# Optimization experiments

Hardware: AMD Instinct MI355X
Metric: run time of the kernel (lower is better)

Reference implementation:

```python
import jax, jax.numpy as jnp
import numpy as np

B, T, C = 2, 2048, 2048
H, HK = 16, 4          # n_head, n_kv_head (GQA)
HD = C // H            # head_dim = 128
EPS = 1e-6             # rms-norm eps


def _rope(x, cos, sin):
    # x: [B,T,h,d]; cos/sin: [T, d/2] (rotate-half RoPE)
    d2 = x.shape[-1] // 2
    x1, x2 = x[..., :d2], x[..., d2:]
    c = cos[None, :, None, :]
    s = sin[None, :, None, :]
    return jnp.concatenate([x1 * c - x2 * s, x1 * s + x2 * c], axis=-1)


def _rms(x):
    # weightless QK-norm (F.rms_norm over last dim)
    return x * jax.lax.rsqrt(jnp.mean(x * x, axis=-1, keepdims=True) + EPS)


def setup_inputs() -> dict:
    key = jax.random.key(0)
    ks = jax.random.split(key, 6)
    x = jax.random.normal(ks[0], (B, T, C), dtype=jnp.float32)
    # realistic RoPE tables
    inv_freq = 1.0 / (10000.0 ** (jnp.arange(0, HD, 2, dtype=jnp.float32) / HD))  # [HD/2]
    ang = jnp.arange(T, dtype=jnp.float32)[:, None] * inv_freq[None, :]           # [T, HD/2]
    cos, sin = jnp.cos(ang), jnp.sin(ang)
    std = 0.02
    Wq = jax.random.normal(ks[1], (C, H * HD), dtype=jnp.float32) * std
    Wk = jax.random.normal(ks[2], (C, HK * HD), dtype=jnp.float32) * std
    Wv = jax.random.normal(ks[3], (C, HK * HD), dtype=jnp.float32) * std
    Wproj = jax.random.normal(ks[4], (C, C), dtype=jnp.float32) * std
    mix1 = jnp.float32(1.0)
    mix2 = jnp.float32(0.5)
    return {"x": x, "cos": cos, "sin": sin, "Wq": Wq, "Wk": Wk, "Wv": Wv,
            "Wproj": Wproj, "mix1": mix1, "mix2": mix2}


def reference(x, cos, sin, Wq, Wk, Wv, Wproj, mix1, mix2):
    Bx, Tx, Cx = x.shape
    q = (x @ Wq).reshape(Bx, Tx, H, HD)
    k = (x @ Wk).reshape(Bx, Tx, HK, HD)
    v = (x @ Wv).reshape(Bx, Tx, HK, HD)
    q = _rms(_rope(q, cos, sin))
    k = _rms(_rope(k, cos, sin))
    q = q.transpose(0, 2, 1, 3)  # [B,H,T,D]
    k = k.transpose(0, 2, 1, 3)  # [B,HK,T,D]
    v = v.transpose(0, 2, 1, 3)
    rep = H // HK
    k = jnp.repeat(k, rep, axis=1)  # GQA repeat -> [B,H,T,D]
    v = jnp.repeat(v, rep, axis=1)
    att = jnp.einsum('bhqd,bhkd->bhqk', q, k) * (1.0 / np.sqrt(HD))
    mask = jnp.tril(jnp.ones((Tx, Tx), dtype=bool))
    att = jnp.where(mask[None, None], att, -jnp.inf)
    att = jax.nn.softmax(att, axis=-1)
    y1 = att @ v            # first-order attention output
    y2 = att @ y1           # second-order simplicial mixing (reuses att)
    y = mix1 * y1 + mix2 * y2
    y = y.transpose(0, 2, 1, 3).reshape(Bx, Tx, Cx)
    return y @ Wproj
```

## Files before the change

### kernel.cpp

```cpp
#include <hip/hip_runtime.h>
#include <hip/hip_bf16.h>
#include <cstdint>
#include <cstddef>

#define AS1 __attribute__((address_space(1)))
#define AS3 __attribute__((address_space(3)))

typedef __attribute__((ext_vector_type(8))) short bf16x8;
typedef __attribute__((ext_vector_type(4))) float f32x4;

__device__ __forceinline__ void gload_lds16(const void* g, void* l) {
  __builtin_amdgcn_global_load_lds((const AS1 void*)g, (AS3 void*)l, 16, 0, 0);
}

#define MFMA_BF16(A, B, C) __builtin_amdgcn_mfma_f32_16x16x32_bf16((A), (B), (C), 0, 0, 0)

#define QSCALE 0.12751744f

__device__ __forceinline__ uint32_t pk2(float a, float b) {
  uint32_t ua = (uint32_t)__builtin_bit_cast(unsigned short, __float2bfloat16(a));
  uint32_t ub = (uint32_t)__builtin_bit_cast(unsigned short, __float2bfloat16(b));
  return ua | (ub << 16);
}
__device__ __forceinline__ float b2f(unsigned short u) {
  return __builtin_bit_cast(float, (uint32_t)u << 16);
}

__device__ __forceinline__ float red8_sum(float v) {
  int x;
  x = __builtin_amdgcn_update_dpp(0, __builtin_bit_cast(int, v), 0xB1, 0xF, 0xF, true);
  v += __builtin_bit_cast(float, x);
  x = __builtin_amdgcn_update_dpp(0, __builtin_bit_cast(int, v), 0x4E, 0xF, 0xF, true);
  v += __builtin_bit_cast(float, x);
  x = __builtin_amdgcn_update_dpp(0, __builtin_bit_cast(int, v), 0x141, 0xF, 0xF, true);
  v += __builtin_bit_cast(float, x);
  return v;
}

__global__ __launch_bounds__(256) void prep_kernel(const float* __restrict__ x,
                                                   __hip_bfloat16* __restrict__ xb,
                                                   const float* __restrict__ Wq,
                                                   const float* __restrict__ Wk,
                                                   const float* __restrict__ Wv,
                                                   const float* __restrict__ Wp,
                                                   __hip_bfloat16* __restrict__ WTa,
                                                   __hip_bfloat16* __restrict__ WpT) {
  __shared__ float tile[32][33];
  int id = blockIdx.x;
  int tx = threadIdx.x, ty = threadIdx.y;
  if (id < 8192) {
    int i = id * 256 + ty * 32 + tx;
    float4 v = ((const float4*)x)[i];
    __hip_bfloat16* o = xb + (size_t)i * 4;
    o[0] = __float2bfloat16(v.x);
    o[1] = __float2bfloat16(v.y);
    o[2] = __float2bfloat16(v.z);
    o[3] = __float2bfloat16(v.w);
    return;
  }
  id -= 8192;
  const float* in; __hip_bfloat16* out; int is, os, bx, by;
  if (id < 4096)      { in = Wq; out = WTa;                          is = 2048; os = 2048; bx = id & 63; by = id >> 6; }
  else if (id < 5120) { int t = id - 4096; in = Wk; out = WTa + (size_t)2048 * 2048; is = 512; os = 2048; bx = t & 15; by = t >> 4; }
  else if (id < 6144) { int t = id - 5120; in = Wv; out = WTa + (size_t)2560 * 2048; is = 512; os = 2048; bx = t & 15; by = t >> 4; }
  else                { int t = id - 6144; in = Wp; out = WpT;       is = 2048; os = 2048; bx = t & 63; by = t >> 6; }
  int c0 = bx * 32, r0 = by * 32;
#pragma unroll
  for (int i = 0; i < 32; i += 8)
    tile[ty + i][tx] = in[(size_t)(r0 + ty + i) * is + c0 + tx];
  __syncthreads();
#pragma unroll
  for (int i = 0; i < 32; i += 8)
    out[(size_t)(c0 + ty + i) * os + r0 + tx] = __float2bfloat16(tile[tx][ty + i]);
}

__global__ __launch_bounds__(256, 2) void gemm_qkv_rope_kernel(
    const __hip_bfloat16* __restrict__ A,
    const __hip_bfloat16* __restrict__ Bt,
    const float* __restrict__ cosb,
    const float* __restrict__ sinb,
    __hip_bfloat16* __restrict__ qT,
    __hip_bfloat16* __restrict__ kT,
    __hip_bfloat16* __restrict__ vt) {
  __shared__ __align__(16) char smem[65536];
  __hip_bfloat16* CL4 = (__hip_bfloat16*)smem;
  const int K = 2048;
  const int tid = threadIdx.x;
  const int lane = tid & 63;
  const int wid = tid >> 6;
  const int wm = wid >> 1, wn = wid & 1;
  const int bid = blockIdx.x;
  const int swz = (bid & 7) * 96 + (bid >> 3);
  const int tm = swz / 24, tn = swz % 24;
  const int row0 = tm << 7, col0 = tn << 7;
  const int fr = lane & 15, hi = lane >> 4;

  auto STAGE = [&](int buf, int k0) {
#pragma unroll
    for (int i = 0; i < 4; ++i) {
      int f = i * 256 + tid;
      int r = f >> 3, s = f & 7, sx = s ^ (r & 7);
      gload_lds16(A + (size_t)(row0 + r) * K + k0 + sx * 8,
                  smem + buf * 16384 + f * 16);
    }
#pragma unroll
    for (int i = 0; i < 4; ++i) {
      int f = i * 256 + tid;
      int r = f >> 3, s = f & 7, sx = s ^ (r & 7);
      gload_lds16(Bt + (size_t)(col0 + r) * K + k0 + sx * 8,
                  smem + 32768 + buf * 16384 + f * 16);
    }
  };

  f32x4 acc[4][4] = {};
  STAGE(0, 0);
  int cur = 0;
  for (int kk = 0; kk < 32; ++kk) {
    if (kk > 0) __builtin_amdgcn_s_barrier();
    __builtin_amdgcn_sched_barrier(0);
    if (kk + 1 < 32) STAGE(cur ^ 1, (kk + 1) * 64);
    __builtin_amdgcn_sched_barrier(0);
    if (kk + 1 < 32) asm volatile("s_waitcnt vmcnt(8)" ::: "memory");
    else             asm volatile("s_waitcnt vmcnt(0)" ::: "memory");
    __builtin_amdgcn_s_barrier();
    __builtin_amdgcn_sched_barrier(0);
    const char* Ac = smem + cur * 16384;
    const char* Bc = smem + 32768 + cur * 16384;
#pragma unroll
    for (int kh = 0; kh < 2; ++kh) {
      bf16x8 af[4], bfr[4];
#pragma unroll
      for (int n = 0; n < 4; ++n) {
        int rowb = wn * 64 + n * 16 + fr;
        int sl = (kh * 4 + hi) ^ (rowb & 7);
        bfr[n] = *(const bf16x8*)(Bc + rowb * 128 + sl * 16);
      }
#pragma unroll
      for (int m = 0; m < 4; ++m) {
        int rowa = wm * 64 + m * 16 + fr;
        int sl = (kh * 4 + hi) ^ (rowa & 7);
        af[m] = *(const bf16x8*)(Ac + rowa * 128 + sl * 16);
      }
      __builtin_amdgcn_s_setprio(1);
#pragma unroll
      for (int m = 0; m < 4; ++m)
#pragma unroll
        for (int n = 0; n < 4; ++n)
          acc[m][n] = MFMA_BF16(af[m], bfr[n], acc[m][n]);
      __builtin_amdgcn_s_setprio(0);
    }
    cur ^= 1;
  }
  __syncthreads();

#pragma unroll
  for (int m = 0; m < 4; ++m)
#pragma unroll
    for (int n = 0; n < 4; ++n) {
      int q4 = wm * 16 + m * 4 + hi;
      int col = wn * 64 + n * 16 + fr;
      *(uint2*)(CL4 + ((q4 * 133 + col) << 2)) =
          make_uint2(pk2(acc[m][n][0], acc[m][n][1]), pk2(acc[m][n][2], acc[m][n][3]));
    }
  __syncthreads();

  const int b = row0 >> 11;
  const int t0 = row0 & 2047;

  if (col0 >= 2560) {
    const int hv = (col0 - 2560) >> 7;
    __hip_bfloat16* vb = vt + (size_t)(b * 4 + hv) * 128 * 2048;
    const int col = tid >> 1, th = tid & 1;
    uint2 w[16];
#pragma unroll
    for (int qq = 0; qq < 16; ++qq)
      w[qq] = *(const uint2*)(CL4 + (((th * 16 + qq) * 133 + col) << 2));
    __hip_bfloat16* dstv = vb + (size_t)col * 2048 + t0 + th * 64;
#pragma unroll
    for (int e = 0; e < 8; ++e)
      *(uint4*)(dstv + e * 8) = make_uint4(w[2 * e].x, w[2 * e].y, w[2 * e + 1].x, w[2 * e + 1].y);
    return;
  }

  const int quad = tid >> 3, cp = tid & 7;
  const int tb = t0 + quad * 4;
  bf16x8 lov[4], hiv[4];
#pragma unroll
  for (int e = 0; e < 4; ++e) {
    lov[e] = *(const bf16x8*)(CL4 + ((quad * 133 + cp * 8 + e * 2) << 2));
    hiv[e] = *(const bf16x8*)(CL4 + ((quad * 133 + 64 + cp * 8 + e * 2) << 2));
  }
  const float oscale = (col0 < 2048) ? QSCALE : 1.0f;
  __hip_bfloat16* dstq = (col0 < 2048)
      ? qT + (size_t)(b * 16 + (col0 >> 7)) * 2048 * 128
      : kT + (size_t)(b * 4 + ((col0 - 2048) >> 7)) * 2048 * 128;

  float o1v[4][8], o2v[4][8], ssum[4];
#pragma unroll
  for (int rr = 0; rr < 4; ++rr) {
    const float* cb = cosb + (size_t)(tb + rr) * 64 + cp * 8;
    const float* sb = sinb + (size_t)(tb + rr) * 64 + cp * 8;
    float4 c0 = *(const float4*)cb, c1 = *(const float4*)(cb + 4);
    float4 s0 = *(const float4*)sb, s1 = *(const float4*)(sb + 4);
    float cc[8] = {c0.x, c0.y, c0.z, c0.w, c1.x, c1.y, c1.z, c1.w};
    float sn[8] = {s0.x, s0.y, s0.z, s0.w, s1.x, s1.y, s1.z, s1.w};
    float ss = 0.f;
#pragma unroll
    for (int e = 0; e < 4; ++e)
#pragma unroll
      for (int w2 = 0; w2 < 2; ++w2) {
        int pd = e * 2 + w2;
        float x1 = b2f((unsigned short)lov[e][w2 * 4 + rr]);
        float x2 = b2f((unsigned short)hiv[e][w2 * 4 + rr]);
        float a = x1 * cc[pd] - x2 * sn[pd];
        float bb = x1 * sn[pd] + x2 * cc[pd];
        o1v[rr][pd] = a;
        o2v[rr][pd] = bb;
        ss += a * a + bb * bb;
      }
    ssum[rr] = ss;
  }
#pragma unroll
  for (int rr = 0; rr < 4; ++rr) {
    float rn = rsqrtf(red8_sum(ssum[rr]) * (1.f / 128.f) + 1e-6f) * oscale;
    __hip_bfloat16* dr = dstq + (size_t)(tb + rr) * 128 + cp * 8;
    *(uint4*)dr = make_uint4(pk2(o1v[rr][0] * rn, o1v[rr][1] * rn),
                             pk2(o1v[rr][2] * rn, o1v[rr][3] * rn),
                             pk2(o1v[rr][4] * rn, o1v[rr][5] * rn),
                             pk2(o1v[rr][6] * rn, o1v[rr][7] * rn));
    *(uint4*)(dr + 64) = make_uint4(pk2(o2v[rr][0] * rn, o2v[rr][1] * rn),
                                    pk2(o2v[rr][2] * rn, o2v[rr][3] * rn),
                                    pk2(o2v[rr][4] * rn, o2v[rr][5] * rn),
                                    pk2(o2v[rr][6] * rn, o2v[rr][7] * rn));
  }
}

__global__ __launch_bounds__(256) void gemm_bf16_kernel(const __hip_bfloat16* __restrict__ A,
                                                        const __hip_bfloat16* __restrict__ Bt,
                                                        float* __restrict__ C,
                                                        int M, int N, int K) {
  __shared__ __align__(16) char smem[32768];
  const int tid = threadIdx.x;
  const int lane = tid & 63;
  const int wid = tid >> 6;
  const int wm = wid >> 1, wn = wid & 1;
  const int nwg = gridDim.x;
  const int bid = blockIdx.x;
  const int swz = (bid & 7) * (nwg >> 3) + (bid >> 3);
  const int ntile = N >> 7;
  const int tm = swz / ntile, tn = swz % ntile;
  const int row0 = tm << 7, col0 = tn << 7;

  const int fr = lane & 15;
  const int kg = (lane >> 4) * 8;

  auto STAGE = [&](int buf, int k0) {
#pragma unroll
    for (int i = 0; i < 2; ++i) {
      int f = i * 256 + tid;
      int r = f >> 2, s = f & 3;
      gload_lds16(A + (size_t)(row0 + r) * K + k0 + s * 8,
                  smem + buf * 8192 + (i * 256 + wid * 64) * 16);
      gload_lds16(Bt + (size_t)(col0 + r) * K + k0 + s * 8,
                  smem + 16384 + buf * 8192 + (i * 256 + wid * 64) * 16);
    }
  };

  f32x4 acc[4][4] = {};
  const int nk = K >> 5;
  STAGE(0, 0);
  int cur = 0;
  for (int kk = 0; kk < nk; ++kk) {
    if (kk > 0) __builtin_amdgcn_s_barrier();
    __builtin_amdgcn_sched_barrier(0);
    if (kk + 1 < nk) STAGE(cur ^ 1, (kk + 1) * 32);
    __builtin_amdgcn_sched_barrier(0);
    if (kk + 1 < nk) asm volatile("s_waitcnt vmcnt(4)" ::: "memory");
    else             asm volatile("s_waitcnt vmcnt(0)" ::: "memory");
    __builtin_amdgcn_s_barrier();
    __builtin_amdgcn_sched_barrier(0);
    const __hip_bfloat16* Ac = (const __hip_bfloat16*)(smem + cur * 8192);
    const __hip_bfloat16* Bc = (const __hip_bfloat16*)(smem + 16384 + cur * 8192);
    bf16x8 af[4], bfr[4];
#pragma unroll
    for (int m = 0; m < 4; ++m)
      af[m] = *(const bf16x8*)(Ac + (wm * 64 + m * 16 + fr) * 32 + kg);
#pragma unroll
    for (int n = 0; n < 4; ++n)
      bfr[n] = *(const bf16x8*)(Bc + (wn * 64 + n * 16 + fr) * 32 + kg);
#pragma unroll
    for (int m = 0; m < 4; ++m)
#pragma unroll
      for (int n = 0; n < 4; ++n)
        acc[m][n] = MFMA_BF16(af[m], bfr[n], acc[m][n]);
    cur ^= 1;
  }

  const int cr = (lane >> 4) * 4;
#pragma unroll
  for (int m = 0; m < 4; ++m)
#pragma unroll
    for (int n = 0; n < 4; ++n) {
      int col = col0 + wn * 64 + n * 16 + fr;
#pragma unroll
      for (int r = 0; r < 4; ++r) {
        int row = row0 + wm * 64 + m * 16 + cr + r;
        C[(size_t)row * N + col] = acc[m][n][r];
      }
    }
}


__global__ __launch_bounds__(256, 2) void attn_pass1_kernel(
    const __hip_bfloat16* __restrict__ qT,
    const __hip_bfloat16* __restrict__ kT,
    const __hip_bfloat16* __restrict__ vt,
    __hip_bfloat16* __restrict__ y1u,
    float* __restrict__ Mb,
    float* __restrict__ Lb,
    const float* __restrict__ mix1p,
    const float* __restrict__ mix2p) {
  __shared__ __align__(16) __hip_bfloat16 Ks[2][64 * 128];
  __shared__ __align__(16) __hip_bfloat16 Vs[2][128 * 64];
  __shared__ __align__(16) char Ps[4][32 * 128];
  const int tid = threadIdx.x, lane = tid & 63, wid = tid >> 6;
  const int bi = blockIdx.x;
  const int u = bi & 255, half = bi >> 8;
  const int g = u & 7;
  const int pslot = (u >> 3) & 7;
  const int bh = g * 4 + (u >> 6);
  const int j = half ? (15 - pslot) : pslot;
  const int q0 = j * 128;
  const int nt = 2 * j + 2;
  const int sd = 2 * j + (wid >> 1);
  const __hip_bfloat16* Kp = kT + (size_t)g * 2048 * 128;
  const __hip_bfloat16* Vp = vt + (size_t)g * 128 * 2048;
  const int fr = lane & 15, hi = lane >> 4;

  bf16x8 qf[2][4];
  {
    const __hip_bfloat16* Qp = qT + ((size_t)bh * 2048 + q0 + wid * 32) * 128;
#pragma unroll
    for (int rr = 0; rr < 2; ++rr)
#pragma unroll
      for (int dc = 0; dc < 4; ++dc)
        qf[rr][dc] = *(const bf16x8*)(Qp + (rr * 16 + fr) * 128 + dc * 32 + hi * 8);
  }

  f32x4 accO[2][8] = {};
  float m[2], l[2];
  m[0] = m[1] = -1e30f; l[0] = l[1] = 0.f;

  char* Pb = Ps[wid];

  auto STAGE = [&](int buf, int kt) {
    const int k0 = kt * 64;
#pragma unroll
    for (int i = 0; i < 4; ++i) {
      int f = i * 256 + tid;
      int r = f >> 4, s = f & 15, sx = s ^ (r & 7);
      gload_lds16(Kp + (size_t)(k0 + r) * 128 + sx * 8,
                  (char*)Ks[buf] + (i * 256 + wid * 64) * 16);
    }
#pragma unroll
    for (int i = 0; i < 4; ++i) {
      int f = i * 256 + tid;
      int r = f >> 3, s = f & 7, sx = s ^ (r & 7);
      gload_lds16(Vp + (size_t)r * 2048 + k0 + sx * 8,
                  (char*)Vs[buf] + (i * 256 + wid * 64) * 16);
    }
  };

  STAGE(0, 0);
  int cur = 0;
  for (int s = 0; s < nt; ++s) {
    if (s > 0) __builtin_amdgcn_s_barrier();
    __builtin_amdgcn_sched_barrier(0);
    if (s + 1 < nt) STAGE(cur ^ 1, s + 1);
    __builtin_amdgcn_sched_barrier(0);
    if (s + 1 < nt) asm volatile("s_waitcnt vmcnt(8)" ::: "memory");
    else            asm volatile("s_waitcnt vmcnt(0)" ::: "memory");
    __builtin_amdgcn_s_barrier();
    __builtin_amdgcn_sched_barrier(0);

    const bool active = (s <= sd);
    if (active) {
      const char* Kc = (const char*)Ks[cur];
      f32x4 sf[2][4] = {};
      __builtin_amdgcn_s_setprio(1);
#pragma unroll
      for (int c = 0; c < 4; ++c) {
        const int krow = c * 16 + fr;
#pragma unroll
        for (int dc = 0; dc < 4; ++dc) {
          int slot = (dc * 4 + hi) ^ (krow & 7);
          bf16x8 kf = *(const bf16x8*)(Kc + krow * 256 + slot * 16);
          sf[0][c] = MFMA_BF16(kf, qf[0][dc], sf[0][c]);
          sf[1][c] = MFMA_BF16(kf, qf[1][dc], sf[1][c]);
        }
      }
      __builtin_amdgcn_s_setprio(0);
      float lmax[2];
#pragma unroll
      for (int rr = 0; rr < 2; ++rr) {
        if (s == sd) {
          const int qq = q0 + wid * 32 + rr * 16 + fr;
#pragma unroll
          for (int c = 0; c < 4; ++c) {
            const int kb = s * 64 + c * 16 + hi * 4;
#pragma unroll
            for (int r = 0; r < 4; ++r)
              if (kb + r > qq) sf[rr][c][r] = -1e30f;
          }
        }
        float v = -1e30f;
#pragma unroll
        for (int c = 0; c < 4; ++c)
#pragma unroll
          for (int r = 0; r < 4; ++r) v = fmaxf(v, sf[rr][c][r]);
        lmax[rr] = v;
      }
      bool grow = (lmax[0] > m[0] + 8.f) | (lmax[1] > m[1] + 8.f);
      if (__any(grow)) {
        float a[2];
#pragma unroll
        for (int rr = 0; rr < 2; ++rr) {
          float v = lmax[rr];
          v = fmaxf(v, __shfl_xor(v, 16));
          v = fmaxf(v, __shfl_xor(v, 32));
          float mn = fmaxf(m[rr], v);
          a[rr] = __builtin_amdgcn_exp2f(m[rr] - mn);
          m[rr] = mn;
          l[rr] *= a[rr];
        }
#pragma unroll
        for (int rr = 0; rr < 2; ++rr)
#pragma unroll
          for (int r = 0; r < 4; ++r) {
            float aq = __shfl(a[rr], hi * 4 + r);
#pragma unroll
            for (int f = 0; f < 8; ++f) accO[rr][f][r] *= aq;
          }
      }
#pragma unroll
      for (int rr = 0; rr < 2; ++rr) {
        float rs = 0.f;
#pragma unroll
        for (int c = 0; c < 4; ++c)
#pragma unroll
          for (int r = 0; r < 4; ++r) {
            float p = __builtin_amdgcn_exp2f(sf[rr][c][r] - m[rr]);
            sf[rr][c][r] = p;
            rs += p;
          }
        l[rr] += rs;
      }
#pragma unroll
      for (int rr = 0; rr < 2; ++rr) {
        const int row = rr * 16 + fr;
        char* Prow = Pb + row * 128;
#pragma unroll
        for (int c = 0; c < 4; ++c) {
          uint32_t w0 = pk2(sf[rr][c][0], sf[rr][c][1]);
          uint32_t w1 = pk2(sf[rr][c][2], sf[rr][c][3]);
          int sl = (c * 2 + (hi >> 1)) ^ (row & 7);
          *(uint2*)(Prow + sl * 16 + (hi & 1) * 8) = make_uint2(w0, w1);
        }
      }
      bf16x8 pf[2][2];
#pragma unroll
      for (int rr = 0; rr < 2; ++rr) {
        const int row = rr * 16 + fr;
#pragma unroll
        for (int kc = 0; kc < 2; ++kc) {
          int sl = (kc * 4 + hi) ^ (row & 7);
          pf[rr][kc] = *(const bf16x8*)(Pb + row * 128 + sl * 16);
        }
      }
      const __hip_bfloat16* Vc = Vs[cur];
      __builtin_amdgcn_s_setprio(1);
#pragma unroll
      for (int kc = 0; kc < 2; ++kc)
#pragma unroll
        for (int f = 0; f < 8; ++f) {
          int vrow = f * 16 + fr;
          int vslot = (kc * 4 + hi) ^ (fr & 7);
          bf16x8 vf = *(const bf16x8*)(Vc + vrow * 64 + vslot * 8);
          accO[0][f] = MFMA_BF16(pf[0][kc], vf, accO[0][f]);
          accO[1][f] = MFMA_BF16(pf[1][kc], vf, accO[1][f]);
        }
      __builtin_amdgcn_s_setprio(0);
    }
    cur ^= 1;
  }

  float lsum[2];
#pragma unroll
  for (int rr = 0; rr < 2; ++rr) {
    float v = l[rr];
    v += __shfl_xor(v, 16);
    v += __shfl_xor(v, 32);
    lsum[rr] = v;
  }
  const float m1v = mix1p[0], m2v = mix2p[0];
  float rlq[2][4];
#pragma unroll
  for (int rr = 0; rr < 2; ++rr) {
    float inv = 1.f / lsum[rr];
#pragma unroll
    for (int r = 0; r < 4; ++r) rlq[rr][r] = __shfl(inv, hi * 4 + r);
  }
  const int t0 = q0 + wid * 32;
#pragma unroll
  for (int rr = 0; rr < 2; ++rr) {
    const int tb = t0 + rr * 16 + hi * 4;
#pragma unroll
    for (int f = 0; f < 8; ++f) {
      const int d = f * 16 + fr;
      const ushort4 v4 = *(const ushort4*)(vt + ((size_t)g * 128 + d) * 2048 + tb);
      float u0 = m1v * b2f(v4.x) + m2v * (accO[rr][f][0] * rlq[rr][0]);
      float u1 = m1v * b2f(v4.y) + m2v * (accO[rr][f][1] * rlq[rr][1]);
      float u2 = m1v * b2f(v4.z) + m2v * (accO[rr][f][2] * rlq[rr][2]);
      float u3 = m1v * b2f(v4.w) + m2v * (accO[rr][f][3] * rlq[rr][3]);
      *(uint2*)(y1u + ((size_t)bh * 128 + d) * 2048 + tb) =
          make_uint2(pk2(u0, u1), pk2(u2, u3));
    }
  }
  if (hi == 0) {
#pragma unroll
    for (int rr = 0; rr < 2; ++rr) {
      Mb[(size_t)bh * 2048 + t0 + rr * 16 + fr] = m[rr];
      Lb[(size_t)bh * 2048 + t0 + rr * 16 + fr] = lsum[rr];
    }
  }
}

__global__ __launch_bounds__(256, 2) void attn_pass2_kernel(
    const __hip_bfloat16* __restrict__ qT,
    const __hip_bfloat16* __restrict__ kT,
    const __hip_bfloat16* __restrict__ y1u,
    const float* __restrict__ Mb,
    const float* __restrict__ Lb,
    __hip_bfloat16* __restrict__ ymix) {
  __shared__ __align__(16) __hip_bfloat16 Ks[2][64 * 128];
  __shared__ __align__(16) __hip_bfloat16 Vs[2][128 * 64];
  __shared__ __align__(16) char Ps[4][32 * 128];
  const int tid = threadIdx.x, lane = tid & 63, wid = tid >> 6;
  const int bi = blockIdx.x;
  const int u = bi & 255, half = bi >> 8;
  const int g = u & 7;
  const int pslot = (u >> 3) & 7;
  const int bh = g * 4 + (u >> 6);
  const int h = bh & 15, b = bh >> 4;
  const int j = half ? (15 - pslot) : pslot;
  const int q0 = j * 128;
  const int nt = 2 * j + 2;
  const int sd = 2 * j + (wid >> 1);
  const __hip_bfloat16* Kp = kT + (size_t)g * 2048 * 128;
  const __hip_bfloat16* Yp = y1u + (size_t)bh * 128 * 2048;
  const int fr = lane & 15, hi = lane >> 4;

  bf16x8 qf[2][4];
  float mr[2], rl[2];
  {
    const __hip_bfloat16* Qp = qT + ((size_t)bh * 2048 + q0 + wid * 32) * 128;
#pragma unroll
    for (int rr = 0; rr < 2; ++rr)
#pragma unroll
      for (int dc = 0; dc < 4; ++dc)
        qf[rr][dc] = *(const bf16x8*)(Qp + (rr * 16 + fr) * 128 + dc * 32 + hi * 8);
    const size_t qb = (size_t)bh * 2048 + q0 + wid * 32;
    mr[0] = Mb[qb + fr];        mr[1] = Mb[qb + 16 + fr];
    rl[0] = 1.f / Lb[qb + fr];  rl[1] = 1.f / Lb[qb + 16 + fr];
  }

  f32x4 accO[2][8] = {};
  char* Pb = Ps[wid];

  auto STAGE = [&](int buf, int kt) {
    const int k0 = kt * 64;
#pragma unroll
    for (int i = 0; i < 4; ++i) {
      int f = i * 256 + tid;
      int r = f >> 4, s = f & 15, sx = s ^ (r & 7);
      gload_lds16(Kp + (size_t)(k0 + r) * 128 + sx * 8,
                  (char*)Ks[buf] + (i * 256 + wid * 64) * 16);
    }
#pragma unroll
    for (int i = 0; i < 4; ++i) {
      int f = i * 256 + tid;
      int r = f >> 3, s = f & 7, sx = s ^ (r & 7);
      gload_lds16(Yp + (size_t)r * 2048 + k0 + sx * 8,
                  (char*)Vs[buf] + (i * 256 + wid * 64) * 16);
    }
  };

  STAGE(0, 0);
  int cur = 0;
  for (int s = 0; s < nt; ++s) {
    if (s > 0) __builtin_amdgcn_s_barrier();
    __builtin_amdgcn_sched_barrier(0);
    if (s + 1 < nt) STAGE(cur ^ 1, s + 1);
    __builtin_amdgcn_sched_barrier(0);
    if (s + 1 < nt) asm volatile("s_waitcnt vmcnt(8)" ::: "memory");
    else            asm volatile("s_waitcnt vmcnt(0)" ::: "memory");
    __builtin_amdgcn_s_barrier();
    __builtin_amdgcn_sched_barrier(0);

    const bool active = (s <= sd);
    if (active) {
      const char* Kc = (const char*)Ks[cur];
      f32x4 sf[2][4] = {};
      __builtin_amdgcn_s_setprio(1);
#pragma unroll
      for (int c = 0; c < 4; ++c) {
        const int krow = c * 16 + fr;
#pragma unroll
        for (int dc = 0; dc < 4; ++dc) {
          int slot = (dc * 4 + hi) ^ (krow & 7);
          bf16x8 kf = *(const bf16x8*)(Kc + krow * 256 + slot * 16);
          sf[0][c] = MFMA_BF16(kf, qf[0][dc], sf[0][c]);
          sf[1][c] = MFMA_BF16(kf, qf[1][dc], sf[1][c]);
        }
      }
      __builtin_amdgcn_s_setprio(0);
#pragma unroll
      for (int rr = 0; rr < 2; ++rr) {
        if (s == sd) {
          const int qq = q0 + wid * 32 + rr * 16 + fr;
#pragma unroll
          for (int c = 0; c < 4; ++c) {
            const int kb = s * 64 + c * 16 + hi * 4;
#pragma unroll
            for (int r = 0; r < 4; ++r)
              if (kb + r > qq) sf[rr][c][r] = -1e30f;
          }
        }
#pragma unroll
        for (int c = 0; c < 4; ++c)
#pragma unroll
          for (int r = 0; r < 4; ++r)
            sf[rr][c][r] = __builtin_amdgcn_exp2f(sf[rr][c][r] - mr[rr]) * rl[rr];
      }
#pragma unroll
      for (int rr = 0; rr < 2; ++rr) {
        const int row = rr * 16 + fr;
        char* Prow = Pb + row * 128;
#pragma unroll
        for (int c = 0; c < 4; ++c) {
          uint32_t w0 = pk2(sf[rr][c][0], sf[rr][c][1]);
          uint32_t w1 = pk2(sf[rr][c][2], sf[rr][c][3]);
          int sl = (c * 2 + (hi >> 1)) ^ (row & 7);
          *(uint2*)(Prow + sl * 16 + (hi & 1) * 8) = make_uint2(w0, w1);
        }
      }
      bf16x8 pf[2][2];
#pragma unroll
      for (int rr = 0; rr < 2; ++rr) {
        const int row = rr * 16 + fr;
#pragma unroll
        for (int kc = 0; kc < 2; ++kc) {
          int sl = (kc * 4 + hi) ^ (row & 7);
          pf[rr][kc] = *(const bf16x8*)(Pb + row * 128 + sl * 16);
        }
      }
      const __hip_bfloat16* Vc = Vs[cur];
      __builtin_amdgcn_s_setprio(1);
#pragma unroll
      for (int kc = 0; kc < 2; ++kc)
#pragma unroll
        for (int f = 0; f < 8; ++f) {
          int vrow = f * 16 + fr;
          int vslot = (kc * 4 + hi) ^ (fr & 7);
          bf16x8 vf = *(const bf16x8*)(Vc + vrow * 64 + vslot * 8);
          accO[0][f] = MFMA_BF16(pf[0][kc], vf, accO[0][f]);
          accO[1][f] = MFMA_BF16(pf[1][kc], vf, accO[1][f]);
        }
      __builtin_amdgcn_s_setprio(0);
    }
    cur ^= 1;
  }

#pragma unroll
  for (int rr = 0; rr < 2; ++rr) {
#pragma unroll
    for (int f = 0; f < 8; ++f) {
      const int d = f * 16 + fr;
#pragma unroll
      for (int r = 0; r < 4; ++r) {
        int q = q0 + wid * 32 + rr * 16 + hi * 4 + r;
        ymix[((size_t)b * 2048 + q) * 2048 + h * 128 + d] = __float2bfloat16(accO[rr][f][r]);
      }
    }
  }
}

extern "C" void kernel_launch(void* const* d_in, const int* in_sizes, int n_in,
                              void* d_out, int out_size, void* d_ws, size_t ws_size,
                              hipStream_t stream) {
  const float* x    = (const float*)d_in[0];
  const float* cosb = (const float*)d_in[1];
  const float* sinb = (const float*)d_in[2];
  const float* Wq   = (const float*)d_in[3];
  const float* Wk   = (const float*)d_in[4];
  const float* Wv   = (const float*)d_in[5];
  const float* Wp   = (const float*)d_in[6];
  const float* mix1 = (const float*)d_in[7];
  const float* mix2 = (const float*)d_in[8];
  float* out = (float*)d_out;
  char* ws = (char*)d_ws;

  __hip_bfloat16* xb   = (__hip_bfloat16*)(ws + 0);
  __hip_bfloat16* WTa  = (__hip_bfloat16*)(ws + 16777216);
  __hip_bfloat16* WpT  = (__hip_bfloat16*)(ws + 29360128);
  __hip_bfloat16* y1u  = (__hip_bfloat16*)(ws + 37748736);
  float*          Mb   = (float*)(ws + 54525952);
  float*          Lb   = (float*)(ws + 54788096);
  __hip_bfloat16* qTb  = (__hip_bfloat16*)(ws + 55050240);
  __hip_bfloat16* kTb  = (__hip_bfloat16*)(ws + 71827456);
  __hip_bfloat16* vtb  = (__hip_bfloat16*)(ws + 76021760);
  __hip_bfloat16* ymix = (__hip_bfloat16*)(ws + 0);

  dim3 tb(32, 8);
  prep_kernel<<<18432, tb, 0, stream>>>(x, xb, Wq, Wk, Wv, Wp, WTa, WpT);

  gemm_qkv_rope_kernel<<<768, 256, 0, stream>>>(xb, WTa, cosb, sinb, qTb, kTb, vtb);

  attn_pass1_kernel<<<512, 256, 0, stream>>>(qTb, kTb, vtb, y1u, Mb, Lb, mix1, mix2);
  attn_pass2_kernel<<<512, 256, 0, stream>>>(qTb, kTb, y1u, Mb, Lb, ymix);

  gemm_bf16_kernel<<<512, 256, 0, stream>>>(ymix, WpT, out, 4096, 2048, 2048);
}
```

Baseline: 243.9 us.

## Software-pipeline QK ahead of softmax/PV in attention; deepen GEMM K-tile with swizzle

Both attention passes now issue the QK^T MFMA for the next key tile before the softmax and PV work of the current tile. K loads are staged two tiles ahead and V one tile ahead, with split staging lambdas and ping-pong score registers. The aim is to overlap matrix-core work with exp/softmax ALU work and hide load latency. Separately, the projection GEMM uses a K-tile of 64 with XOR-swizzled LDS, 64KB shared memory and launch bounds of 2 blocks per CU. This halves barrier count per K and reduces bank conflicts, at the cost of more LDS and register pressure. The unrolled-by-two loop assumes nt is even.

```diff
diff --git a/kernel.cpp b/kernel.cpp
--- a/kernel.cpp
+++ b/kernel.cpp
@@ -235,11 +235,11 @@
   }
 }
 
-__global__ __launch_bounds__(256) void gemm_bf16_kernel(const __hip_bfloat16* __restrict__ A,
-                                                        const __hip_bfloat16* __restrict__ Bt,
-                                                        float* __restrict__ C,
-                                                        int M, int N, int K) {
-  __shared__ __align__(16) char smem[32768];
+__global__ __launch_bounds__(256, 2) void gemm_bf16_kernel(const __hip_bfloat16* __restrict__ A,
+                                                           const __hip_bfloat16* __restrict__ Bt,
+                                                           float* __restrict__ C,
+                                                           int M, int N, int K) {
+  __shared__ __align__(16) char smem[65536];
   const int tid = threadIdx.x;
   const int lane = tid & 63;
   const int wid = tid >> 6;
@@ -250,53 +250,67 @@
   const int ntile = N >> 7;
   const int tm = swz / ntile, tn = swz % ntile;
   const int row0 = tm << 7, col0 = tn << 7;
-
-  const int fr = lane & 15;
-  const int kg = (lane >> 4) * 8;
+  const int fr = lane & 15, hi = lane >> 4;
 
   auto STAGE = [&](int buf, int k0) {
 #pragma unroll
-    for (int i = 0; i < 2; ++i) {
+    for (int i = 0; i < 4; ++i) {
       int f = i * 256 + tid;
-      int r = f >> 2, s = f & 3;
-      gload_lds16(A + (size_t)(row0 + r) * K + k0 + s * 8,
-                  smem + buf * 8192 + (i * 256 + wid * 64) * 16);
-      gload_lds16(Bt + (size_t)(col0 + r) * K + k0 + s * 8,
-                  smem + 16384 + buf * 8192 + (i * 256 + wid * 64) * 16);
+      int r = f >> 3, s = f & 7, sx = s ^ (r & 7);
+      gload_lds16(A + (size_t)(row0 + r) * K + k0 + sx * 8,
+                  smem + buf * 16384 + f * 16);
+    }
+#pragma unroll
+    for (int i = 0; i < 4; ++i) {
+      int f = i * 256 + tid;
+      int r = f >> 3, s = f & 7, sx = s ^ (r & 7);
+      gload_lds16(Bt + (size_t)(col0 + r) * K + k0 + sx * 8,
+                  smem + 32768 + buf * 16384 + f * 16);
     }
   };
 
   f32x4 acc[4][4] = {};
-  const int nk = K >> 5;
+  const int nk = K >> 6;
   STAGE(0, 0);
   int cur = 0;
   for (int kk = 0; kk < nk; ++kk) {
     if (kk > 0) __builtin_amdgcn_s_barrier();
     __builtin_amdgcn_sched_barrier(0);
-    if (kk + 1 < nk) STAGE(cur ^ 1, (kk + 1) * 32);
-    __builtin_amdgcn_sched_barrier(0);
-    if (kk + 1 < nk) asm volatile("s_waitcnt vmcnt(4)" ::: "memory");
+    if (kk + 1 < nk) STAGE(cur ^ 1, (kk + 1) * 64);
+    __builtin_amdgcn_sched_barrier(0);
+    if (kk + 1 < nk) asm volatile("s_waitcnt vmcnt(8)" ::: "memory");
     else             asm volatile("s_waitcnt vmcnt(0)" ::: "memory");
     __builtin_amdgcn_s_barrier();
     __builtin_amdgcn_sched_barrier(0);
-    const __hip_bfloat16* Ac = (const __hip_bfloat16*)(smem + cur * 8192);
-    const __hip_bfloat16* Bc = (const __hip_bfloat16*)(smem + 16384 + cur * 8192);
-    bf16x8 af[4], bfr[4];
-#pragma unroll
-    for (int m = 0; m < 4; ++m)
-      af[m] = *(const bf16x8*)(Ac + (wm * 64 + m * 16 + fr) * 32 + kg);
-#pragma unroll
-    for (int n = 0; n < 4; ++n)
-      bfr[n] = *(const bf16x8*)(Bc + (wn * 64 + n * 16 + fr) * 32 + kg);
-#pragma unroll
-    for (int m = 0; m < 4; ++m)
-#pragma unroll
-      for (int n = 0; n < 4; ++n)
-        acc[m][n] = MFMA_BF16(af[m], bfr[n], acc[m][n]);
+    const char* Ac = smem + cur * 16384;
+    const char* Bc = smem + 32768 + cur * 16384;
+#pragma unroll
+    for (int kh = 0; kh < 2; ++kh) {
+      bf16x8 af[4], bfr[4];
+#pragma unroll
+      for (int n = 0; n < 4; ++n) {
+        int rowb = wn * 64 + n * 16 + fr;
+        int sl = (kh * 4 + hi) ^ (rowb & 7);
+        bfr[n] = *(const bf16x8*)(Bc + rowb * 128 + sl * 16);
+      }
+#pragma unroll
+      for (int m = 0; m < 4; ++m) {
+        int rowa = wm * 64 + m * 16 + fr;
+        int sl = (kh * 4 + hi) ^ (rowa & 7);
+        af[m] = *(const bf16x8*)(Ac + rowa * 128 + sl * 16);
+      }
+      __builtin_amdgcn_s_setprio(1);
+#pragma unroll
+      for (int m = 0; m < 4; ++m)
+#pragma unroll
+        for (int n = 0; n < 4; ++n)
+          acc[m][n] = MFMA_BF16(af[m], bfr[n], acc[m][n]);
+      __builtin_amdgcn_s_setprio(0);
+    }
     cur ^= 1;
   }
 
-  const int cr = (lane >> 4) * 4;
+  const int cr = hi * 4;
 #pragma unroll
   for (int m = 0; m < 4; ++m)
 #pragma unroll
@@ -353,7 +367,7 @@
 
   char* Pb = Ps[wid];
 
-  auto STAGE = [&](int buf, int kt) {
+  auto STAGE_K = [&](int buf, int kt) {
     const int k0 = kt * 64;
 #pragma unroll
     for (int i = 0; i < 4; ++i) {
@@ -362,6 +376,9 @@
       gload_lds16(Kp + (size_t)(k0 + r) * 128 + sx * 8,
                   (char*)Ks[buf] + (i * 256 + wid * 64) * 16);
     }
+  };
+  auto STAGE_V = [&](int buf, int kt) {
+    const int k0 = kt * 64;
 #pragma unroll
     for (int i = 0; i < 4; ++i) {
       int f = i * 256 + tid;
@@ -371,35 +388,42 @@
     }
   };
 
-  STAGE(0, 0);
-  int cur = 0;
-  for (int s = 0; s < nt; ++s) {
-    if (s > 0) __builtin_amdgcn_s_barrier();
-    __builtin_amdgcn_sched_barrier(0);
-    if (s + 1 < nt) STAGE(cur ^ 1, s + 1);
-    __builtin_amdgcn_sched_barrier(0);
-    if (s + 1 < nt) asm volatile("s_waitcnt vmcnt(8)" ::: "memory");
-    else            asm volatile("s_waitcnt vmcnt(0)" ::: "memory");
+  auto QK = [&](int t, f32x4 (&sf)[2][4]) {
+    const char* Kc = (const char*)Ks[t & 1];
+#pragma unroll
+    for (int rr = 0; rr < 2; ++rr)
+#pragma unroll
+      for (int c = 0; c < 4; ++c) sf[rr][c] = (f32x4){0.f, 0.f, 0.f, 0.f};
+    __builtin_amdgcn_s_setprio(1);
+#pragma unroll
+    for (int c = 0; c < 4; ++c) {
+      const int krow = c * 16 + fr;
+#pragma unroll
+      for (int dc = 0; dc < 4; ++dc) {
+        int slot = (dc * 4 + hi) ^ (krow & 7);
+        bf16x8 kf = *(const bf16x8*)(Kc + krow * 256 + slot * 16);
+        sf[0][c] = MFMA_BF16(kf, qf[0][dc], sf[0][c]);
+        sf[1][c] = MFMA_BF16(kf, qf[1][dc], sf[1][c]);
+      }
+    }
+    __builtin_amdgcn_s_setprio(0);
+  };
+
+  auto STEP = [&](int s, f32x4 (&sfC)[2][4], f32x4 (&sfN)[2][4]) {
     __builtin_amdgcn_s_barrier();
     __builtin_amdgcn_sched_barrier(0);
-
-    const bool active = (s <= sd);
-    if (active) {
-      const char* Kc = (const char*)Ks[cur];
-      f32x4 sf[2][4] = {};
-      __builtin_amdgcn_s_setprio(1);
-#pragma unroll
-      for (int c = 0; c < 4; ++c) {
-        const int krow = c * 16 + fr;
-#pragma unroll
-        for (int dc = 0; dc < 4; ++dc) {
-          int slot = (dc * 4 + hi) ^ (krow & 7);
-          bf16x8 kf = *(const bf16x8*)(Kc + krow * 256 + slot * 16);
-          sf[0][c] = MFMA_BF16(kf, qf[0][dc], sf[0][c]);
-          sf[1][c] = MFMA_BF16(kf, qf[1][dc], sf[1][c]);
-        }
-      }
-      __builtin_amdgcn_s_setprio(0);
+    if (s + 2 < nt) STAGE_K(s & 1, s + 2);
+    if (s + 1 < nt) STAGE_V((s + 1) & 1, s + 1);
+    __builtin_amdgcn_sched_barrier(0);
+    if (s + 2 < nt)      asm volatile("s_waitcnt vmcnt(8)" ::: "memory");
+    else if (s + 1 < nt) asm volatile("s_waitcnt vmcnt(4)" ::: "memory");
+    else                 asm volatile("s_waitcnt vmcnt(0)" ::: "memory");
+    __builtin_amdgcn_s_barrier();
+    __builtin_amdgcn_sched_barrier(0);
+
+    if (s + 1 <= sd) QK(s + 1, sfN);
+
+    if (s <= sd) {
       float lmax[2];
 #pragma unroll
       for (int rr = 0; rr < 2; ++rr) {
@@ -410,14 +434,14 @@
             const int kb = s * 64 + c * 16 + hi * 4;
 #pragma unroll
             for (int r = 0; r < 4; ++r)
-              if (kb + r > qq) sf[rr][c][r] = -1e30f;
+              if (kb + r > qq) sfC[rr][c][r] = -1e30f;
           }
         }
         float v = -1e30f;
 #pragma unroll
         for (int c = 0; c < 4; ++c)
 #pragma unroll
-          for (int r = 0; r < 4; ++r) v = fmaxf(v, sf[rr][c][r]);
+          for (int r = 0; r < 4; ++r) v = fmaxf(v, sfC[rr][c][r]);
         lmax[rr] = v;
       }
       bool grow = (lmax[0] > m[0] + 8.f) | (lmax[1] > m[1] + 8.f);
@@ -449,8 +473,8 @@
         for (int c = 0; c < 4; ++c)
 #pragma unroll
           for (int r = 0; r < 4; ++r) {
-            float p = __builtin_amdgcn_exp2f(sf[rr][c][r] - m[rr]);
-            sf[rr][c][r] = p;
+            float p = __builtin_amdgcn_exp2f(sfC[rr][c][r] - m[rr]);
+            sfC[rr][c][r] = p;
             rs += p;
           }
         l[rr] += rs;
@@ -461,8 +485,8 @@
         char* Prow = Pb + row * 128;
 #pragma unroll
         for (int c = 0; c < 4; ++c) {
-          uint32_t w0 = pk2(sf[rr][c][0], sf[rr][c][1]);
-          uint32_t w1 = pk2(sf[rr][c][2], sf[rr][c][3]);
+          uint32_t w0 = pk2(sfC[rr][c][0], sfC[rr][c][1]);
+          uint32_t w1 = pk2(sfC[rr][c][2], sfC[rr][c][3]);
           int sl = (c * 2 + (hi >> 1)) ^ (row & 7);
           *(uint2*)(Prow + sl * 16 + (hi & 1) * 8) = make_uint2(w0, w1);
         }
@@ -477,7 +501,7 @@
           pf[rr][kc] = *(const bf16x8*)(Pb + row * 128 + sl * 16);
         }
       }
-      const __hip_bfloat16* Vc = Vs[cur];
+      const __hip_bfloat16* Vc = Vs[s & 1];
       __builtin_amdgcn_s_setprio(1);
 #pragma unroll
       for (int kc = 0; kc < 2; ++kc)
@@ -491,7 +515,20 @@
         }
       __builtin_amdgcn_s_setprio(0);
     }
-    cur ^= 1;
+  };
+
+  f32x4 sfA[2][4], sfB[2][4];
+  STAGE_K(0, 0);
+  STAGE_V(0, 0);
+  STAGE_K(1, 1);
+  asm volatile("s_waitcnt vmcnt(8)" ::: "memory");
+  __builtin_amdgcn_s_barrier();
+  __builtin_amdgcn_sched_barrier(0);
+  QK(0, sfA);
+
+  for (int s2 = 0; s2 < nt; s2 += 2) {
+    STEP(s2, sfA, sfB);
+    STEP(s2 + 1, sfB, sfA);
   }
 
   float lsum[2];
@@ -577,7 +614,7 @@
   f32x4 accO[2][8] = {};
   char* Pb = Ps[wid];
 
-  auto STAGE = [&](int buf, int kt) {
+  auto STAGE_K = [&](int buf, int kt) {
     const int k0 = kt * 64;
 #pragma unroll
     for (int i = 0; i < 4; ++i) {
@@ -586,6 +623,9 @@
       gload_lds16(Kp + (size_t)(k0 + r) * 128 + sx * 8,
                   (char*)Ks[buf] + (i * 256 + wid * 64) * 16);
     }
+  };
+  auto STAGE_V = [&](int buf, int kt) {
+    const int k0 = kt * 64;
 #pragma unroll
     for (int i = 0; i < 4; ++i) {
       int f = i * 256 + tid;
@@ -595,35 +635,42 @@
     }
   };
 
-  STAGE(0, 0);
-  int cur = 0;
-  for (int s = 0; s < nt; ++s) {
-    if (s > 0) __builtin_amdgcn_s_barrier();
-    __builtin_amdgcn_sched_barrier(0);
-    if (s + 1 < nt) STAGE(cur ^ 1, s + 1);
-    __builtin_amdgcn_sched_barrier(0);
-    if (s + 1 < nt) asm volatile("s_waitcnt vmcnt(8)" ::: "memory");
-    else            asm volatile("s_waitcnt vmcnt(0)" ::: "memory");
+  auto QK = [&](int t, f32x4 (&sf)[2][4]) {
+    const char* Kc = (const char*)Ks[t & 1];
+#pragma unroll
+    for (int rr = 0; rr < 2; ++rr)
+#pragma unroll
+      for (int c = 0; c < 4; ++c) sf[rr][c] = (f32x4){0.f, 0.f, 0.f, 0.f};
+    __builtin_amdgcn_s_setprio(1);
+#pragma unroll
+    for (int c = 0; c < 4; ++c) {
+      const int krow = c * 16 + fr;
+#pragma unroll
+      for (int dc = 0; dc < 4; ++dc) {
+        int slot = (dc * 4 + hi) ^ (krow & 7);
+        bf16x8 kf = *(const bf16x8*)(Kc + krow * 256 + slot * 16);
+        sf[0][c] = MFMA_BF16(kf, qf[0][dc], sf[0][c]);
+        sf[1][c] = MFMA_BF16(kf, qf[1][dc], sf[1][c]);
+      }
+    }
+    __builtin_amdgcn_s_setprio(0);
+  };
+
+  auto STEP = [&](int s, f32x4 (&sfC)[2][4], f32x4 (&sfN)[2][4]) {
     __builtin_amdgcn_s_barrier();
     __builtin_amdgcn_sched_barrier(0);
-
-    const bool active = (s <= sd);
-    if (active) {
-      const char* Kc = (const char*)Ks[cur];
-      f32x4 sf[2][4] = {};
-      __builtin_amdgcn_s_setprio(1);
-#pragma unroll
-      for (int c = 0; c < 4; ++c) {
-        const int krow = c * 16 + fr;
-#pragma unroll
-        for (int dc = 0; dc < 4; ++dc) {
-          int slot = (dc * 4 + hi) ^ (krow & 7);
-          bf16x8 kf = *(const bf16x8*)(Kc + krow * 256 + slot * 16);
-          sf[0][c] = MFMA_BF16(kf, qf[0][dc], sf[0][c]);
-          sf[1][c] = MFMA_BF16(kf, qf[1][dc], sf[1][c]);
-        }
-      }
-      __builtin_amdgcn_s_setprio(0);
+    if (s + 2 < nt) STAGE_K(s & 1, s + 2);
+    if (s + 1 < nt) STAGE_V((s + 1) & 1, s + 1);
+    __builtin_amdgcn_sched_barrier(0);
+    if (s + 2 < nt)      asm volatile("s_waitcnt vmcnt(8)" ::: "memory");
+    else if (s + 1 < nt) asm volatile("s_waitcnt vmcnt(4)" ::: "memory");
+    else                 asm volatile("s_waitcnt vmcnt(0)" ::: "memory");
+    __builtin_amdgcn_s_barrier();
+    __builtin_amdgcn_sched_barrier(0);
+
+    if (s + 1 <= sd) QK(s + 1, sfN);
+
+    if (s <= sd) {
 #pragma unroll
       for (int rr = 0; rr < 2; ++rr) {
         if (s == sd) {
@@ -633,14 +680,14 @@
             const int kb = s * 64 + c * 16 + hi * 4;
 #pragma unroll
             for (int r = 0; r < 4; ++r)
-              if (kb + r > qq) sf[rr][c][r] = -1e30f;
+              if (kb + r > qq) sfC[rr][c][r] = -1e30f;
           }
         }
 #pragma unroll
         for (int c = 0; c < 4; ++c)
 #pragma unroll
           for (int r = 0; r < 4; ++r)
-            sf[rr][c][r] = __builtin_amdgcn_exp2f(sf[rr][c][r] - mr[rr]) * rl[rr];
+            sfC[rr][c][r] = __builtin_amdgcn_exp2f(sfC[rr][c][r] - mr[rr]) * rl[rr];
       }
 #pragma unroll
       for (int rr = 0; rr < 2; ++rr) {
@@ -648,8 +695,8 @@
         char* Prow = Pb + row * 128;
 #pragma unroll
         for (int c = 0; c < 4; ++c) {
-          uint32_t w0 = pk2(sf[rr][c][0], sf[rr][c][1]);
-          uint32_t w1 = pk2(sf[rr][c][2], sf[rr][c][3]);
+          uint32_t w0 = pk2(sfC[rr][c][0], sfC[rr][c][1]);
+          uint32_t w1 = pk2(sfC[rr][c][2], sfC[rr][c][3]);
           int sl = (c * 2 + (hi >> 1)) ^ (row & 7);
           *(uint2*)(Prow + sl * 16 + (hi & 1) * 8) = make_uint2(w0, w1);
         }
@@ -664,7 +711,7 @@
           pf[rr][kc] = *(const bf16x8*)(Pb + row * 128 + sl * 16);
         }
       }
-      const __hip_bfloat16* Vc = Vs[cur];
+      const __hip_bfloat16* Vc = Vs[s & 1];
       __builtin_amdgcn_s_setprio(1);
 #pragma unroll
       for (int kc = 0; kc < 2; ++kc)
@@ -678,7 +725,20 @@
         }
       __builtin_amdgcn_s_setprio(0);
     }
-    cur ^= 1;
+  };
+
+  f32x4 sfA[2][4], sfB[2][4];
+  STAGE_K(0, 0);
+  STAGE_V(0, 0);
+  STAGE_K(1, 1);
+  asm volatile("s_waitcnt vmcnt(8)" ::: "memory");
+  __builtin_amdgcn_s_barrier();
+  __builtin_amdgcn_sched_barrier(0);
+  QK(0, sfA);
+
+  for (int s2 = 0; s2 < nt; s2 += 2) {
+    STEP(s2, sfA, sfB);
+    STEP(s2 + 1, sfB, sfA);
   }
 
 #pragma unroll
```

Measured after the change: 237.5 us. 1.03x faster.
